# Optimization experiments

Hardware: AMD Instinct MI355X
Metric: run time of the kernel (lower is better)

Reference implementation:

```python
import jax, jax.numpy as jnp
import numpy as np

B, N, F, U = 4, 4096, 256, 128
NEG = -1.0e9


def setup_inputs() -> dict:
    key = jax.random.key(0)
    k1, k2, k3, k4, k5 = jax.random.split(key, 5)
    inputs = jax.random.normal(k1, (B, N, F), dtype=jnp.float32)
    # Glorot-normal-like scales
    w = jax.random.normal(k2, (F, U), dtype=jnp.float32) * np.sqrt(2.0 / (F + U)).astype(np.float32)
    ai = jax.random.normal(k3, (U, N), dtype=jnp.float32) * np.sqrt(2.0 / (U + N)).astype(np.float32)
    aj = jax.random.normal(k4, (U, N), dtype=jnp.float32) * np.sqrt(2.0 / (U + N)).astype(np.float32)
    a = (jax.random.uniform(k5, (N, N)) < 0.004).astype(jnp.float32)
    adj = jnp.maximum(a, a.T)
    return {"inputs": inputs, "w": w, "ai": ai, "aj": aj, "adj": adj}


def reference(inputs, w, ai, aj, adj):
    # f: [B, N, U]
    f = jnp.einsum('bnf,fu->bnu', inputs, w)
    # self_attn[b,i,j] = (f ai)[b,i,j]; other_attn = transpose([0,2,1]) of (f aj)
    self_attn = jnp.einsum('bnu,um->bnm', f, ai)          # [B, N, N]
    other_attn = jnp.einsum('bnu,um->bmn', f, aj)         # transposed [B, N, N]
    mask = adj + jnp.eye(N, dtype=adj.dtype)              # allow self + neighbors
    attn = self_attn + other_attn + NEG * (1.0 - mask)
    attn = jax.nn.softmax(attn, axis=1)                   # softmax over rows (axis=1)
    # out[b,j,u] = sum_i f[b,i,u] * attn[b,i,j]
    out = jnp.einsum('biu,bij->bju', f, attn)
    return jax.nn.relu(out), attn
```

## Files before the change

kernel.cpp:

```cpp
#include <hip/hip_runtime.h>
#include <hip/hip_bf16.h>

#define NN 4096
#define UU 128
#define BB 4
#define FF 256
#define MAXD 128

__global__ __launch_bounds__(256) void transpose2(const float* __restrict__ ai,
                                                  const float* __restrict__ aj,
                                                  float* __restrict__ aiT,
                                                  float* __restrict__ ajT) {
    __shared__ float tile[32][33];
    const float* src = blockIdx.z ? aj : ai;
    float* dst = blockIdx.z ? ajT : aiT;
    int n0 = blockIdx.x * 32;
    int u0 = blockIdx.y * 32;
    int tx = threadIdx.x;
    int ty = threadIdx.y;
    for (int r = 0; r < 32; r += 8)
        tile[ty + r][tx] = src[(size_t)(u0 + ty + r) * NN + n0 + tx];
    __syncthreads();
    for (int r = 0; r < 32; r += 8)
        dst[(size_t)(n0 + ty + r) * UU + u0 + tx] = tile[tx][ty + r];
}

__global__ __launch_bounds__(256) void fgemm(const float* __restrict__ A,
                                             const float* __restrict__ Wm,
                                             float* __restrict__ F) {
    __shared__ float As[16][68];
    __shared__ float Bs[16][64];
    int tid = threadIdx.x;
    int tx = tid & 15, ty = tid >> 4;
    int row0 = blockIdx.x * 64;
    int col0 = blockIdx.y * 64;
    float acc[4][4] = {};
    for (int kb = 0; kb < FF; kb += 16) {
        int r = tid >> 2, kq = (tid & 3) << 2;
        const float4 av = *(const float4*)(A + (size_t)(row0 + r) * FF + kb + kq);
        As[kq + 0][r] = av.x; As[kq + 1][r] = av.y;
        As[kq + 2][r] = av.z; As[kq + 3][r] = av.w;
        int k = tid >> 4, nq = (tid & 15) << 2;
        *(float4*)&Bs[k][nq] = *(const float4*)(Wm + (size_t)(kb + k) * UU + col0 + nq);
        __syncthreads();
#pragma unroll
        for (int kk = 0; kk < 16; kk++) {
            float4 a4 = *(const float4*)&As[kk][ty * 4];
            float4 b4 = *(const float4*)&Bs[kk][tx * 4];
            acc[0][0] += a4.x * b4.x; acc[0][1] += a4.x * b4.y; acc[0][2] += a4.x * b4.z; acc[0][3] += a4.x * b4.w;
            acc[1][0] += a4.y * b4.x; acc[1][1] += a4.y * b4.y; acc[1][2] += a4.y * b4.z; acc[1][3] += a4.y * b4.w;
            acc[2][0] += a4.z * b4.x; acc[2][1] += a4.z * b4.y; acc[2][2] += a4.z * b4.z; acc[2][3] += a4.z * b4.w;
            acc[3][0] += a4.w * b4.x; acc[3][1] += a4.w * b4.y; acc[3][2] += a4.w * b4.z; acc[3][3] += a4.w * b4.w;
        }
        __syncthreads();
    }
#pragma unroll
    for (int ii = 0; ii < 4; ii++) {
        *(float4*)(F + (size_t)(row0 + ty * 4 + ii) * UU + col0 + tx * 4) =
            make_float4(acc[ii][0], acc[ii][1], acc[ii][2], acc[ii][3]);
    }
}

__global__ __launch_bounds__(256) void scan_adj(const float* __restrict__ adj,
                                                unsigned short* __restrict__ csc,
                                                int* __restrict__ cnt,
                                                int* __restrict__ dblf) {
    __shared__ unsigned short tmp[MAXD];
    __shared__ int c, d;
    int j = blockIdx.x, tid = threadIdx.x;
    if (tid == 0) { c = 0; d = 0; }
    __syncthreads();
    const float4* row = (const float4*)(adj + (size_t)j * NN);
#pragma unroll
    for (int k = 0; k < 4; k++) {
        int q = tid + k * 256;
        float4 v = row[q];
        int base = q * 4;
        float vals[4] = {v.x, v.y, v.z, v.w};
#pragma unroll
        for (int t = 0; t < 4; t++) {
            int i = base + t;
            bool nz = (vals[t] != 0.0f);
            if (i == j) { if (nz) d = 1; nz = true; }
            if (nz) {
                int p = atomicAdd(&c, 1);
                if (p < MAXD) tmp[p] = (unsigned short)i;
            }
        }
    }
    __syncthreads();
    int M = c < MAXD ? c : MAXD;
    if (tid < M) csc[(size_t)j * MAXD + tid] = tmp[tid];
    if (tid == 0) { cnt[j] = M; dblf[j] = d; }
}

__global__ __launch_bounds__(256) void gat_cols(const unsigned short* __restrict__ csc,
                                                const int* __restrict__ cnt,
                                                const int* __restrict__ dblf,
                                                const float* __restrict__ f,
                                                const float* __restrict__ aiT,
                                                const float* __restrict__ ajT,
                                                float* __restrict__ out,
                                                float* __restrict__ attn) {
    __shared__ unsigned short sidx[MAXD];
    __shared__ float sex[BB][MAXD];
    int j = blockIdx.x, tid = threadIdx.x;
    int lane = tid & 63, b = tid >> 6;
    int M = cnt[j];
    int oneh = dblf[j];
    if (tid < M) sidx[tid] = csc[(size_t)j * MAXD + tid];

    const float* fb = f + (size_t)b * NN * UU;
    float2 fj = *(const float2*)(fb + (size_t)j * UU + 2 * lane);

    if (oneh) {
        if (lane == 0) attn[((size_t)(b * NN + j)) * NN + j] = 1.0f;
        float2 o;
        o.x = fj.x > 0.0f ? fj.x : 0.0f;
        o.y = fj.y > 0.0f ? fj.y : 0.0f;
        *(float2*)(out + ((size_t)(b * NN + j)) * UU + 2 * lane) = o;
        return;
    }
    __syncthreads();

    float2 ai2 = *(const float2*)(aiT + (size_t)j * UU + 2 * lane);
    float denom = 0.0f, acc0 = 0.0f, acc1 = 0.0f;
    for (int e = 0; e < M; e++) {
        int i = sidx[e];
        float2 fi  = *(const float2*)(fb + (size_t)i * UU + 2 * lane);
        float2 aj2 = *(const float2*)(ajT + (size_t)i * UU + 2 * lane);
        float p = fi.x * ai2.x + fi.y * ai2.y + fj.x * aj2.x + fj.y * aj2.y;
#pragma unroll
        for (int off = 32; off > 0; off >>= 1) p += __shfl_xor(p, off);
        float ex = __expf(p);
        denom += ex;
        acc0 += ex * fi.x;
        acc1 += ex * fi.y;
        if (lane == 0) sex[b][e] = ex;
    }
    float inv = 1.0f / denom;

    float2 o;
    o.x = acc0 * inv; o.y = acc1 * inv;
    o.x = o.x > 0.0f ? o.x : 0.0f;
    o.y = o.y > 0.0f ? o.y : 0.0f;
    *(float2*)(out + ((size_t)(b * NN + j)) * UU + 2 * lane) = o;

    __syncthreads();
    for (int e = lane; e < M; e += 64)
        attn[((size_t)(b * NN + sidx[e])) * NN + j] = sex[b][e] * inv;
}

extern "C" void kernel_launch(void* const* d_in, const int* in_sizes, int n_in,
                              void* d_out, int out_size, void* d_ws, size_t ws_size,
                              hipStream_t stream) {
    const float* inputs = (const float*)d_in[0];
    const float* w      = (const float*)d_in[1];
    const float* ai     = (const float*)d_in[2];
    const float* aj     = (const float*)d_in[3];
    const float* adj    = (const float*)d_in[4];

    float* out  = (float*)d_out;
    float* attn = out + (size_t)BB * NN * UU;

    float* f   = (float*)d_ws;
    float* aiT = f + (size_t)BB * NN * UU;
    float* ajT = aiT + (size_t)NN * UU;
    unsigned short* csc = (unsigned short*)(ajT + (size_t)NN * UU);
    int* cnt  = (int*)(csc + (size_t)NN * MAXD);
    int* dblf = cnt + NN;

    hipMemsetAsync(attn, 0, (size_t)BB * NN * NN * sizeof(float), stream);

    transpose2<<<dim3(NN / 32, UU / 32, 2), dim3(32, 8), 0, stream>>>(ai, aj, aiT, ajT);
    fgemm<<<dim3((BB * NN) / 64, UU / 64), 256, 0, stream>>>(inputs, w, f);
    scan_adj<<<NN, 256, 0, stream>>>(adj, csc, cnt, dblf);
    gat_cols<<<NN, 256, 0, stream>>>(csc, cnt, dblf, f, aiT, ajT, out, attn);
}
```

Baseline: 442.5 us.

## Unroll GAT edge loop, keep exp values in registers, simplify fgemm

```diff
diff --git a/kernel.cpp b/kernel.cpp
--- a/kernel.cpp
+++ b/kernel.cpp
@@ -28,37 +28,33 @@
 __global__ __launch_bounds__(256) void fgemm(const float* __restrict__ A,
                                              const float* __restrict__ Wm,
                                              float* __restrict__ F) {
-    __shared__ float As[16][68];
-    __shared__ float Bs[16][64];
     int tid = threadIdx.x;
-    int tx = tid & 15, ty = tid >> 4;
-    int row0 = blockIdx.x * 64;
-    int col0 = blockIdx.y * 64;
-    float acc[4][4] = {};
-    for (int kb = 0; kb < FF; kb += 16) {
-        int r = tid >> 2, kq = (tid & 3) << 2;
-        const float4 av = *(const float4*)(A + (size_t)(row0 + r) * FF + kb + kq);
-        As[kq + 0][r] = av.x; As[kq + 1][r] = av.y;
-        As[kq + 2][r] = av.z; As[kq + 3][r] = av.w;
-        int k = tid >> 4, nq = (tid & 15) << 2;
-        *(float4*)&Bs[k][nq] = *(const float4*)(Wm + (size_t)(kb + k) * UU + col0 + nq);
-        __syncthreads();
+    int cg = tid & 3;
+    int r = tid >> 2;
+    int row = blockIdx.x * 64 + r;
+    int c0 = blockIdx.y * 32 + cg * 8;
+
+    const float* arow = A + (size_t)row * FF;
+    const float* wp = Wm + c0;
+    float4 acc0 = {0, 0, 0, 0}, acc1 = {0, 0, 0, 0};
+#pragma unroll 4
+    for (int kb = 0; kb < FF; kb += 4) {
+        float4 a4 = *(const float4*)(arow + kb);
+        float av[4] = {a4.x, a4.y, a4.z, a4.w};
 #pragma unroll
-        for (int kk = 0; kk < 16; kk++) {
-            float4 a4 = *(const float4*)&As[kk][ty * 4];
-            float4 b4 = *(const float4*)&Bs[kk][tx * 4];
-            acc[0][0] += a4.x * b4.x; acc[0][1] += a4.x * b4.y; acc[0][2] += a4.x * b4.z; acc[0][3] += a4.x * b4.w;
-            acc[1][0] += a4.y * b4.x; acc[1][1] += a4.y * b4.y; acc[1][2] += a4.y * b4.z; acc[1][3] += a4.y * b4.w;
-            acc[2][0] += a4.z * b4.x; acc[2][1] += a4.z * b4.y; acc[2][2] += a4.z * b4.z; acc[2][3] += a4.z * b4.w;
-            acc[3][0] += a4.w * b4.x; acc[3][1] += a4.w * b4.y; acc[3][2] += a4.w * b4.z; acc[3][3] += a4.w * b4.w;
+        for (int t = 0; t < 4; t++) {
+            const float* wrow = wp + (size_t)(kb + t) * UU;
+            float4 w0 = *(const float4*)(wrow);
+            float4 w1 = *(const float4*)(wrow + 4);
+            acc0.x += av[t] * w0.x; acc0.y += av[t] * w0.y;
+            acc0.z += av[t] * w0.z; acc0.w += av[t] * w0.w;
+            acc1.x += av[t] * w1.x; acc1.y += av[t] * w1.y;
+            acc1.z += av[t] * w1.z; acc1.w += av[t] * w1.w;
         }
-        __syncthreads();
-    }
-#pragma unroll
-    for (int ii = 0; ii < 4; ii++) {
-        *(float4*)(F + (size_t)(row0 + ty * 4 + ii) * UU + col0 + tx * 4) =
-            make_float4(acc[ii][0], acc[ii][1], acc[ii][2], acc[ii][3]);
-    }
+    }
+    float* frow = F + (size_t)row * UU + c0;
+    *(float4*)(frow) = acc0;
+    *(float4*)(frow + 4) = acc1;
 }
 
 __global__ __launch_bounds__(256) void scan_adj(const float* __restrict__ adj,
@@ -103,12 +99,11 @@
                                                 float* __restrict__ out,
                                                 float* __restrict__ attn) {
     __shared__ unsigned short sidx[MAXD];
-    __shared__ float sex[BB][MAXD];
     int j = blockIdx.x, tid = threadIdx.x;
     int lane = tid & 63, b = tid >> 6;
     int M = cnt[j];
     int oneh = dblf[j];
-    if (tid < M) sidx[tid] = csc[(size_t)j * MAXD + tid];
+    if (tid < MAXD) sidx[tid] = csc[(size_t)j * MAXD + tid];
 
     const float* fb = f + (size_t)b * NN * UU;
     float2 fj = *(const float2*)(fb + (size_t)j * UU + 2 * lane);
@@ -125,19 +120,44 @@
 
     float2 ai2 = *(const float2*)(aiT + (size_t)j * UU + 2 * lane);
     float denom = 0.0f, acc0 = 0.0f, acc1 = 0.0f;
-    for (int e = 0; e < M; e++) {
+    float keep0 = 0.0f, keep1 = 0.0f;
+
+#define EDGE(ee, fi, aj2v)                                                    \
+    {                                                                         \
+        float p = fi.x * ai2.x + fi.y * ai2.y + fj.x * aj2v.x + fj.y * aj2v.y;\
+        _Pragma("unroll")                                                     \
+        for (int off = 32; off > 0; off >>= 1) p += __shfl_xor(p, off);       \
+        float ex = __expf(p);                                                 \
+        denom += ex;                                                          \
+        acc0 += ex * fi.x;                                                    \
+        acc1 += ex * fi.y;                                                    \
+        if (((ee) & 63) == lane) { if ((ee) < 64) keep0 = ex; else keep1 = ex; } \
+    }
+
+    int e = 0;
+    for (; e + 4 <= M; e += 4) {
+        int i0 = sidx[e], i1 = sidx[e + 1], i2 = sidx[e + 2], i3 = sidx[e + 3];
+        float2 f0 = *(const float2*)(fb + (size_t)i0 * UU + 2 * lane);
+        float2 a0 = *(const float2*)(ajT + (size_t)i0 * UU + 2 * lane);
+        float2 f1 = *(const float2*)(fb + (size_t)i1 * UU + 2 * lane);
+        float2 a1 = *(const float2*)(ajT + (size_t)i1 * UU + 2 * lane);
+        float2 f2 = *(const float2*)(fb + (size_t)i2 * UU + 2 * lane);
+        float2 a2 = *(const float2*)(ajT + (size_t)i2 * UU + 2 * lane);
+        float2 f3 = *(const float2*)(fb + (size_t)i3 * UU + 2 * lane);
+        float2 a3 = *(const float2*)(ajT + (size_t)i3 * UU + 2 * lane);
+        EDGE(e, f0, a0);
+        EDGE(e + 1, f1, a1);
+        EDGE(e + 2, f2, a2);
+        EDGE(e + 3, f3, a3);
+    }
+    for (; e < M; e++) {
         int i = sidx[e];
-        float2 fi  = *(const float2*)(fb + (size_t)i * UU + 2 * lane);
-        float2 aj2 = *(const float2*)(ajT + (size_t)i * UU + 2 * lane);
-        float p = fi.x * ai2.x + fi.y * ai2.y + fj.x * aj2.x + fj.y * aj2.y;
-#pragma unroll
-        for (int off = 32; off > 0; off >>= 1) p += __shfl_xor(p, off);
-        float ex = __expf(p);
-        denom += ex;
-        acc0 += ex * fi.x;
-        acc1 += ex * fi.y;
-        if (lane == 0) sex[b][e] = ex;
-    }
+        float2 fi = *(const float2*)(fb + (size_t)i * UU + 2 * lane);
+        float2 av = *(const float2*)(ajT + (size_t)i * UU + 2 * lane);
+        EDGE(e, fi, av);
+    }
+#undef EDGE
+
     float inv = 1.0f / denom;
 
     float2 o;
@@ -146,9 +166,10 @@
     o.y = o.y > 0.0f ? o.y : 0.0f;
     *(float2*)(out + ((size_t)(b * NN + j)) * UU + 2 * lane) = o;
 
-    __syncthreads();
-    for (int e = lane; e < M; e += 64)
-        attn[((size_t)(b * NN + sidx[e])) * NN + j] = sex[b][e] * inv;
+    if (lane < M)
+        attn[((size_t)(b * NN + sidx[lane])) * NN + j] = keep0 * inv;
+    if (lane + 64 < M)
+        attn[((size_t)(b * NN + sidx[lane + 64])) * NN + j] = keep1 * inv;
 }
 
 extern "C" void kernel_launch(void* const* d_in, const int* in_sizes, int n_in,
@@ -173,7 +194,7 @@
     hipMemsetAsync(attn, 0, (size_t)BB * NN * NN * sizeof(float), stream);
 
     transpose2<<<dim3(NN / 32, UU / 32, 2), dim3(32, 8), 0, stream>>>(ai, aj, aiT, ajT);
-    fgemm<<<dim3((BB * NN) / 64, UU / 64), 256, 0, stream>>>(inputs, w, f);
+    fgemm<<<dim3((BB * NN) / 64, UU / 32), 256, 0, stream>>>(inputs, w, f);
     scan_adj<<<NN, 256, 0, stream>>>(adj, csc, cnt, dblf);
     gat_cols<<<NN, 256, 0, stream>>>(csc, cnt, dblf, f, aiT, ajT, out, attn);
 }
```

After: 498.9 us. +12.7%, slower.
